# Optimization experiments

Measured on AMD Instinct MI355X. Metric: run time of the kernel, lower is better.

## Reference

```python
import jax, jax.numpy as jnp
import numpy as np

NEG = -1000000000.0

def setup_inputs() -> dict:
    key = jax.random.key(0)
    k1, k2, k3, k4 = jax.random.split(key, 4)
    B, S, D = 8, 4096, 256
    query = jax.random.normal(k1, (B, S, D), dtype=jnp.float32)
    k_ = jax.random.normal(k2, (B, S, D), dtype=jnp.float32)
    value = jax.random.normal(k3, (B, S, D), dtype=jnp.float32)
    mask = jax.random.bernoulli(k4, 0.1, (B, S, 1))  # True = masked
    return {"query": query, "key": k_, "value": value, "mask": mask}

def reference(query, key, value, mask):
    # a: [B,S,1] sum of squares of query; b: [B,S,1] for key
    a = jnp.sum(query * query, axis=-1, keepdims=True)
    b = jnp.sum(key * key, axis=-1, keepdims=True)
    # s1 = (K^T / b) @ V  -> [B, D, D]; divide each key row s by b_s
    s1 = jnp.einsum('bsd,bse->bde', key / b, value)
    # score = Q / a, masked rows set to -1e9
    score = query / a
    score = jnp.where(mask, NEG, score)
    s2 = jnp.einsum('bsd,bde->bse', score, s1)
    return s2 / query.shape[-1]
```

## Files before the change

kernel.cpp:

```cpp
#include <hip/hip_runtime.h>

#define BB 8
#define SS 4096
#define DD 256
#define NEGV -1000000000.0f

typedef float f32x4 __attribute__((ext_vector_type(4)));
typedef short s16x8 __attribute__((ext_vector_type(8)));

static __device__ __forceinline__ unsigned short f2bf(float x) {
  unsigned int u = __builtin_bit_cast(unsigned int, x);
  u += 0x7fffu + ((u >> 16) & 1u);
  return (unsigned short)(u >> 16);
}

__global__ __launch_bounds__(256) void prep_kernel(
    const float* __restrict__ Q, const float* __restrict__ K,
    const float* __restrict__ V, const int* __restrict__ mask,
    unsigned short* __restrict__ QS, unsigned short* __restrict__ KT,
    unsigned short* __restrict__ VT) {
  __shared__ unsigned short tile[DD * 68];
  const int b = blockIdx.y;
  const int s_base = blockIdx.x * 64;
  const int tid = threadIdx.x;
  const int w = tid >> 6;
  const int l = tid & 63;

  for (int it = 0; it < 16; ++it) {
    const int s = s_base + w * 16 + it;
    const size_t rowo = ((size_t)b * SS + s) * DD;
    const float4 q = *(const float4*)(Q + rowo + l * 4);
    float ss = q.x * q.x + q.y * q.y + q.z * q.z + q.w * q.w;
#pragma unroll
    for (int off = 32; off; off >>= 1) ss += __shfl_xor(ss, off);
    const int m = mask[b * SS + s];
    const float ca = m ? 0.0f : (1.0f / ss);
    const float aa = m ? NEGV : 0.0f;
    ushort4 o;
    o.x = f2bf(q.x * ca + aa);
    o.y = f2bf(q.y * ca + aa);
    o.z = f2bf(q.z * ca + aa);
    o.w = f2bf(q.w * ca + aa);
    *(ushort4*)(QS + rowo + l * 4) = o;
  }

  for (int it = 0; it < 16; ++it) {
    const int sl = w * 16 + it;
    const int s = s_base + sl;
    const float4 k = *(const float4*)(K + ((size_t)b * SS + s) * DD + l * 4);
    float ss = k.x * k.x + k.y * k.y + k.z * k.z + k.w * k.w;
#pragma unroll
    for (int off = 32; off; off >>= 1) ss += __shfl_xor(ss, off);
    const float binv = 1.0f / ss;
    tile[(l * 4 + 0) * 68 + sl] = f2bf(k.x * binv);
    tile[(l * 4 + 1) * 68 + sl] = f2bf(k.y * binv);
    tile[(l * 4 + 2) * 68 + sl] = f2bf(k.z * binv);
    tile[(l * 4 + 3) * 68 + sl] = f2bf(k.w * binv);
  }
  __syncthreads();
  {
    const size_t base = ((size_t)b * DD + tid) * SS + s_base;
#pragma unroll
    for (int c = 0; c < 8; ++c) {
      const uint2 a = *(const uint2*)(tile + tid * 68 + c * 8);
      const uint2 b2 = *(const uint2*)(tile + tid * 68 + c * 8 + 4);
      uint4 vv;
      vv.x = a.x; vv.y = a.y; vv.z = b2.x; vv.w = b2.y;
      *(uint4*)(KT + base + c * 8) = vv;
    }
  }
  __syncthreads();

  for (int it = 0; it < 16; ++it) {
    const int sl = w * 16 + it;
    const int s = s_base + sl;
    const float4 v = *(const float4*)(V + ((size_t)b * SS + s) * DD + l * 4);
    tile[(l * 4 + 0) * 68 + sl] = f2bf(v.x);
    tile[(l * 4 + 1) * 68 + sl] = f2bf(v.y);
    tile[(l * 4 + 2) * 68 + sl] = f2bf(v.z);
    tile[(l * 4 + 3) * 68 + sl] = f2bf(v.w);
  }
  __syncthreads();
  {
    const size_t base = ((size_t)b * DD + tid) * SS + s_base;
#pragma unroll
    for (int c = 0; c < 8; ++c) {
      const uint2 a = *(const uint2*)(tile + tid * 68 + c * 8);
      const uint2 b2 = *(const uint2*)(tile + tid * 68 + c * 8 + 4);
      uint4 vv;
      vv.x = a.x; vv.y = a.y; vv.z = b2.x; vv.w = b2.y;
      *(uint4*)(VT + base + c * 8) = vv;
    }
  }
}

__global__ __launch_bounds__(256) void p2_kernel(
    const unsigned short* __restrict__ KT, const unsigned short* __restrict__ VT,
    float* __restrict__ s1T) {
  __shared__ unsigned short vt_l[128 * 40];
  __shared__ unsigned short kt_l[128 * 40];
  const int b = blockIdx.z;
  const int d0 = (blockIdx.x & 1) * 128;
  const int e0 = (blockIdx.x >> 1) * 128;
  const int sbeg = blockIdx.y * 512;
  const int tid = threadIdx.x;
  const int w = tid >> 6, l = tid & 63;
  const int wr = w & 1, wc = w >> 1;
  const int quad = l >> 4, mr = l & 15;

  f32x4 acc[4][4];
#pragma unroll
  for (int i = 0; i < 4; ++i)
#pragma unroll
    for (int j = 0; j < 4; ++j) acc[i][j] = (f32x4){0.f, 0.f, 0.f, 0.f};

  const size_t vbase = ((size_t)b * DD + e0) * SS;
  const size_t kbase = ((size_t)b * DD + d0) * SS;

  for (int ks = 0; ks < 16; ++ks) {
    const int sc = sbeg + ks * 32;
#pragma unroll
    for (int it = 0; it < 2; ++it) {
      const int flat = it * 256 + tid;
      const int row = flat >> 2;
      const int c8 = (flat & 3) * 8;
      *(uint4*)(vt_l + row * 40 + c8) =
          *(const uint4*)(VT + vbase + (size_t)row * SS + sc + c8);
      *(uint4*)(kt_l + row * 40 + c8) =
          *(const uint4*)(KT + kbase + (size_t)row * SS + sc + c8);
    }
    __syncthreads();
    s16x8 af[4], bfr[4];
#pragma unroll
    for (int i = 0; i < 4; ++i)
      af[i] = *(const s16x8*)(vt_l + (wr * 64 + i * 16 + mr) * 40 + quad * 8);
#pragma unroll
    for (int j = 0; j < 4; ++j)
      bfr[j] = *(const s16x8*)(kt_l + (wc * 64 + j * 16 + mr) * 40 + quad * 8);
#pragma unroll
    for (int i = 0; i < 4; ++i)
#pragma unroll
      for (int j = 0; j < 4; ++j)
        acc[i][j] = __builtin_amdgcn_mfma_f32_16x16x32_bf16(af[i], bfr[j],
                                                            acc[i][j], 0, 0, 0);
    __syncthreads();
  }

#pragma unroll
  for (int i = 0; i < 4; ++i) {
    const int e = e0 + wr * 64 + i * 16 + quad * 4;
#pragma unroll
    for (int j = 0; j < 4; ++j) {
      const int d = d0 + wc * 64 + j * 16 + mr;
      float* p = s1T + ((size_t)b * DD + e) * DD + d;
#pragma unroll
      for (int r = 0; r < 4; ++r) atomicAdd(p + (size_t)r * DD, acc[i][j][r]);
    }
  }
}

__global__ __launch_bounds__(256) void p3_kernel(
    const unsigned short* __restrict__ QS, const float* __restrict__ s1T,
    float* __restrict__ out) {
  __shared__ unsigned short qs_l[128 * 40];
  __shared__ unsigned short s1_l[128 * 40];
  const int b = blockIdx.z;
  const int e0 = blockIdx.x * 128;
  const int s0 = blockIdx.y * 128;
  const int tid = threadIdx.x;
  const int w = tid >> 6, l = tid & 63;
  const int wr = w & 1, wc = w >> 1;
  const int quad = l >> 4, mr = l & 15;

  f32x4 acc[4][4];
#pragma unroll
  for (int i = 0; i < 4; ++i)
#pragma unroll
    for (int j = 0; j < 4; ++j) acc[i][j] = (f32x4){0.f, 0.f, 0.f, 0.f};

  for (int ks = 0; ks < 8; ++ks) {
    const int dc = ks * 32;
#pragma unroll
    for (int it = 0; it < 2; ++it) {
      const int flat = it * 256 + tid;
      const int row = flat >> 2;
      const int c8 = (flat & 3) * 8;
      *(uint4*)(qs_l + row * 40 + c8) =
          *(const uint4*)(QS + ((size_t)b * SS + s0 + row) * DD + dc + c8);
    }
#pragma unroll
    for (int it = 0; it < 4; ++it) {
      const int flat = it * 256 + tid;
      const int row = flat >> 3;
      const int c4 = (flat & 7) * 4;
      const float4 sv =
          *(const float4*)(s1T + ((size_t)b * DD + e0 + row) * DD + dc + c4);
      ushort4 o;
      o.x = f2bf(sv.x); o.y = f2bf(sv.y); o.z = f2bf(sv.z); o.w = f2bf(sv.w);
      *(ushort4*)(s1_l + row * 40 + c4) = o;
    }
    __syncthreads();
    s16x8 af[4], bfr[4];
#pragma unroll
    for (int i = 0; i < 4; ++i)
      af[i] = *(const s16x8*)(qs_l + (wr * 64 + i * 16 + mr) * 40 + quad * 8);
#pragma unroll
    for (int j = 0; j < 4; ++j)
      bfr[j] = *(const s16x8*)(s1_l + (wc * 64 + j * 16 + mr) * 40 + quad * 8);
#pragma unroll
    for (int i = 0; i < 4; ++i)
#pragma unroll
      for (int j = 0; j < 4; ++j)
        acc[i][j] = __builtin_amdgcn_mfma_f32_16x16x32_bf16(af[i], bfr[j],
                                                            acc[i][j], 0, 0, 0);
    __syncthreads();
  }

#pragma unroll
  for (int i = 0; i < 4; ++i) {
    const int s = s0 + wr * 64 + i * 16 + quad * 4;
#pragma unroll
    for (int j = 0; j < 4; ++j) {
      const int e = e0 + wc * 64 + j * 16 + mr;
      float* p = out + ((size_t)b * SS + s) * DD + e;
#pragma unroll
      for (int r = 0; r < 4; ++r) p[(size_t)r * DD] = acc[i][j][r] * (1.0f / DD);
    }
  }
}

extern "C" void kernel_launch(void* const* d_in, const int* in_sizes, int n_in,
                              void* d_out, int out_size, void* d_ws,
                              size_t ws_size, hipStream_t stream) {
  const float* Q = (const float*)d_in[0];
  const float* K = (const float*)d_in[1];
  const float* V = (const float*)d_in[2];
  const int* mask = (const int*)d_in[3];
  float* out = (float*)d_out;

  char* ws = (char*)d_ws;
  const size_t MB16 = (size_t)16 * 1024 * 1024;
  unsigned short* QS = (unsigned short*)(ws);
  unsigned short* KT = (unsigned short*)(ws + MB16);
  unsigned short* VT = (unsigned short*)(ws + 2 * MB16);
  float* s1T = (float*)(ws + 3 * MB16);

  hipMemsetAsync(s1T, 0, (size_t)BB * DD * DD * sizeof(float), stream);
  prep_kernel<<<dim3(SS / 64, BB), 256, 0, stream>>>(Q, K, V, mask, QS, KT, VT);
  p2_kernel<<<dim3(4, 8, BB), 256, 0, stream>>>(KT, VT, s1T);
  p3_kernel<<<dim3(2, SS / 128, BB), 256, 0, stream>>>(QS, s1T, out);
}
```

Measured before the change: 193.2 us.

## Split prep across Q/K/V blocks, replace atomics with split-K partials and reduce

```diff
diff --git a/kernel.cpp b/kernel.cpp
--- a/kernel.cpp
+++ b/kernel.cpp
@@ -19,90 +19,77 @@
     const float* __restrict__ V, const int* __restrict__ mask,
     unsigned short* __restrict__ QS, unsigned short* __restrict__ KT,
     unsigned short* __restrict__ VT) {
-  __shared__ unsigned short tile[DD * 68];
+  __shared__ unsigned short tile[DD * 34];
   const int b = blockIdx.y;
-  const int s_base = blockIdx.x * 64;
+  const int s0 = blockIdx.x * 32;
   const int tid = threadIdx.x;
-  const int w = tid >> 6;
-  const int l = tid & 63;
-
-  for (int it = 0; it < 16; ++it) {
-    const int s = s_base + w * 16 + it;
-    const size_t rowo = ((size_t)b * SS + s) * DD;
-    const float4 q = *(const float4*)(Q + rowo + l * 4);
-    float ss = q.x * q.x + q.y * q.y + q.z * q.z + q.w * q.w;
+  const int w = tid >> 6, l = tid & 63;
+
+  if (blockIdx.z == 0) {
+#pragma unroll
+    for (int it = 0; it < 8; ++it) {
+      const int s = s0 + w * 8 + it;
+      const size_t rowo = ((size_t)b * SS + s) * DD;
+      const float4 q = *(const float4*)(Q + rowo + l * 4);
+      float ss = q.x * q.x + q.y * q.y + q.z * q.z + q.w * q.w;
+#pragma unroll
+      for (int off = 32; off; off >>= 1) ss += __shfl_xor(ss, off);
+      const int m = mask[b * SS + s];
+      const float ca = m ? 0.0f : (1.0f / ss);
+      const float aa = m ? NEGV : 0.0f;
+      ushort4 o;
+      o.x = f2bf(q.x * ca + aa);
+      o.y = f2bf(q.y * ca + aa);
+      o.z = f2bf(q.z * ca + aa);
+      o.w = f2bf(q.w * ca + aa);
+      *(ushort4*)(QS + rowo + l * 4) = o;
+    }
+    return;
+  }
+
+  const int isK = (blockIdx.z == 1);
+  const float* __restrict__ src = isK ? K : V;
+  unsigned short* __restrict__ dst = isK ? KT : VT;
+
+#pragma unroll
+  for (int it = 0; it < 8; ++it) {
+    const int sl = w * 8 + it;
+    const size_t rowo = ((size_t)b * SS + s0 + sl) * DD;
+    const float v0 = src[rowo + l];
+    const float v1 = src[rowo + l + 64];
+    const float v2 = src[rowo + l + 128];
+    const float v3 = src[rowo + l + 192];
+    float ss = v0 * v0 + v1 * v1 + v2 * v2 + v3 * v3;
 #pragma unroll
     for (int off = 32; off; off >>= 1) ss += __shfl_xor(ss, off);
-    const int m = mask[b * SS + s];
-    const float ca = m ? 0.0f : (1.0f / ss);
-    const float aa = m ? NEGV : 0.0f;
-    ushort4 o;
-    o.x = f2bf(q.x * ca + aa);
-    o.y = f2bf(q.y * ca + aa);
-    o.z = f2bf(q.z * ca + aa);
-    o.w = f2bf(q.w * ca + aa);
-    *(ushort4*)(QS + rowo + l * 4) = o;
-  }
-
-  for (int it = 0; it < 16; ++it) {
-    const int sl = w * 16 + it;
-    const int s = s_base + sl;
-    const float4 k = *(const float4*)(K + ((size_t)b * SS + s) * DD + l * 4);
-    float ss = k.x * k.x + k.y * k.y + k.z * k.z + k.w * k.w;
-#pragma unroll
-    for (int off = 32; off; off >>= 1) ss += __shfl_xor(ss, off);
-    const float binv = 1.0f / ss;
-    tile[(l * 4 + 0) * 68 + sl] = f2bf(k.x * binv);
-    tile[(l * 4 + 1) * 68 + sl] = f2bf(k.y * binv);
-    tile[(l * 4 + 2) * 68 + sl] = f2bf(k.z * binv);
-    tile[(l * 4 + 3) * 68 + sl] = f2bf(k.w * binv);
+    const float sc = isK ? (1.0f / ss) : 1.0f;
+    tile[(l) * 34 + sl] = f2bf(v0 * sc);
+    tile[(l + 64) * 34 + sl] = f2bf(v1 * sc);
+    tile[(l + 128) * 34 + sl] = f2bf(v2 * sc);
+    tile[(l + 192) * 34 + sl] = f2bf(v3 * sc);
   }
   __syncthreads();
-  {
-    const size_t base = ((size_t)b * DD + tid) * SS + s_base;
-#pragma unroll
-    for (int c = 0; c < 8; ++c) {
-      const uint2 a = *(const uint2*)(tile + tid * 68 + c * 8);
-      const uint2 b2 = *(const uint2*)(tile + tid * 68 + c * 8 + 4);
-      uint4 vv;
-      vv.x = a.x; vv.y = a.y; vv.z = b2.x; vv.w = b2.y;
-      *(uint4*)(KT + base + c * 8) = vv;
-    }
-  }
-  __syncthreads();
-
-  for (int it = 0; it < 16; ++it) {
-    const int sl = w * 16 + it;
-    const int s = s_base + sl;
-    const float4 v = *(const float4*)(V + ((size_t)b * SS + s) * DD + l * 4);
-    tile[(l * 4 + 0) * 68 + sl] = f2bf(v.x);
-    tile[(l * 4 + 1) * 68 + sl] = f2bf(v.y);
-    tile[(l * 4 + 2) * 68 + sl] = f2bf(v.z);
-    tile[(l * 4 + 3) * 68 + sl] = f2bf(v.w);
-  }
-  __syncthreads();
-  {
-    const size_t base = ((size_t)b * DD + tid) * SS + s_base;
-#pragma unroll
-    for (int c = 0; c < 8; ++c) {
-      const uint2 a = *(const uint2*)(tile + tid * 68 + c * 8);
-      const uint2 b2 = *(const uint2*)(tile + tid * 68 + c * 8 + 4);
-      uint4 vv;
-      vv.x = a.x; vv.y = a.y; vv.z = b2.x; vv.w = b2.y;
-      *(uint4*)(VT + base + c * 8) = vv;
-    }
+  const size_t base = ((size_t)b * DD + tid) * SS + s0;
+#pragma unroll
+  for (int c = 0; c < 4; ++c) {
+    uint4 vv;
+    vv.x = *(const unsigned int*)(tile + tid * 34 + c * 8 + 0);
+    vv.y = *(const unsigned int*)(tile + tid * 34 + c * 8 + 2);
+    vv.z = *(const unsigned int*)(tile + tid * 34 + c * 8 + 4);
+    vv.w = *(const unsigned int*)(tile + tid * 34 + c * 8 + 6);
+    *(uint4*)(dst + base + c * 8) = vv;
   }
 }
 
 __global__ __launch_bounds__(256) void p2_kernel(
     const unsigned short* __restrict__ KT, const unsigned short* __restrict__ VT,
-    float* __restrict__ s1T) {
+    float* __restrict__ part, int nks) {
   __shared__ unsigned short vt_l[128 * 40];
   __shared__ unsigned short kt_l[128 * 40];
   const int b = blockIdx.z;
   const int d0 = (blockIdx.x & 1) * 128;
   const int e0 = (blockIdx.x >> 1) * 128;
-  const int sbeg = blockIdx.y * 512;
+  const int sbeg = blockIdx.y * nks * 32;
   const int tid = threadIdx.x;
   const int w = tid >> 6, l = tid & 63;
   const int wr = w & 1, wc = w >> 1;
@@ -117,7 +104,7 @@
   const size_t vbase = ((size_t)b * DD + e0) * SS;
   const size_t kbase = ((size_t)b * DD + d0) * SS;
 
-  for (int ks = 0; ks < 16; ++ks) {
+  for (int ks = 0; ks < nks; ++ks) {
     const int sc = sbeg + ks * 32;
 #pragma unroll
     for (int it = 0; it < 2; ++it) {
@@ -146,21 +133,36 @@
     __syncthreads();
   }
 
+  float* pb = part + (((size_t)blockIdx.y * BB + b) * DD) * DD;
 #pragma unroll
   for (int i = 0; i < 4; ++i) {
     const int e = e0 + wr * 64 + i * 16 + quad * 4;
 #pragma unroll
     for (int j = 0; j < 4; ++j) {
       const int d = d0 + wc * 64 + j * 16 + mr;
-      float* p = s1T + ((size_t)b * DD + e) * DD + d;
-#pragma unroll
-      for (int r = 0; r < 4; ++r) atomicAdd(p + (size_t)r * DD, acc[i][j][r]);
-    }
-  }
+      float* p = pb + (size_t)e * DD + d;
+#pragma unroll
+      for (int r = 0; r < 4; ++r) p[(size_t)r * DD] = acc[i][j][r];
+    }
+  }
+}
+
+__global__ __launch_bounds__(256) void reduce_kernel(
+    const float* __restrict__ part, unsigned short* __restrict__ s1b,
+    int split) {
+  const size_t i4 = ((size_t)blockIdx.x * 256 + threadIdx.x) * 4;
+  float ax = 0.f, ay = 0.f, az = 0.f, aw = 0.f;
+  for (int p = 0; p < split; ++p) {
+    const float4 v = *(const float4*)(part + (size_t)p * (BB * DD * DD) + i4);
+    ax += v.x; ay += v.y; az += v.z; aw += v.w;
+  }
+  ushort4 o;
+  o.x = f2bf(ax); o.y = f2bf(ay); o.z = f2bf(az); o.w = f2bf(aw);
+  *(ushort4*)(s1b + i4) = o;
 }
 
 __global__ __launch_bounds__(256) void p3_kernel(
-    const unsigned short* __restrict__ QS, const float* __restrict__ s1T,
+    const unsigned short* __restrict__ QS, const unsigned short* __restrict__ s1b,
     float* __restrict__ out) {
   __shared__ unsigned short qs_l[128 * 40];
   __shared__ unsigned short s1_l[128 * 40];
@@ -187,17 +189,8 @@
       const int c8 = (flat & 3) * 8;
       *(uint4*)(qs_l + row * 40 + c8) =
           *(const uint4*)(QS + ((size_t)b * SS + s0 + row) * DD + dc + c8);
-    }
-#pragma unroll
-    for (int it = 0; it < 4; ++it) {
-      const int flat = it * 256 + tid;
-      const int row = flat >> 3;
-      const int c4 = (flat & 7) * 4;
-      const float4 sv =
-          *(const float4*)(s1T + ((size_t)b * DD + e0 + row) * DD + dc + c4);
-      ushort4 o;
-      o.x = f2bf(sv.x); o.y = f2bf(sv.y); o.z = f2bf(sv.z); o.w = f2bf(sv.w);
-      *(ushort4*)(s1_l + row * 40 + c4) = o;
+      *(uint4*)(s1_l + row * 40 + c8) =
+          *(const uint4*)(s1b + ((size_t)b * DD + e0 + row) * DD + dc + c8);
     }
     __syncthreads();
     s16x8 af[4], bfr[4];
@@ -239,14 +232,20 @@
   float* out = (float*)d_out;
 
   char* ws = (char*)d_ws;
-  const size_t MB16 = (size_t)16 * 1024 * 1024;
+  const size_t MB = (size_t)1024 * 1024;
   unsigned short* QS = (unsigned short*)(ws);
-  unsigned short* KT = (unsigned short*)(ws + MB16);
-  unsigned short* VT = (unsigned short*)(ws + 2 * MB16);
-  float* s1T = (float*)(ws + 3 * MB16);
-
-  hipMemsetAsync(s1T, 0, (size_t)BB * DD * DD * sizeof(float), stream);
-  prep_kernel<<<dim3(SS / 64, BB), 256, 0, stream>>>(Q, K, V, mask, QS, KT, VT);
-  p2_kernel<<<dim3(4, 8, BB), 256, 0, stream>>>(KT, VT, s1T);
-  p3_kernel<<<dim3(2, SS / 128, BB), 256, 0, stream>>>(QS, s1T, out);
-}
+  unsigned short* KT = (unsigned short*)(ws + 16 * MB);
+  unsigned short* VT = (unsigned short*)(ws + 32 * MB);
+  float* part = (float*)(ws + 48 * MB);
+
+  const int split = (ws_size >= (size_t)84 * MB) ? 16 : 8;
+  const int nks = SS / (32 * split);
+  unsigned short* s1b =
+      (unsigned short*)(ws + 48 * MB + (size_t)split * 2 * MB);
+
+  prep_kernel<<<dim3(SS / 32, BB, 3), 256, 0, stream>>>(Q, K, V, mask, QS, KT,
+                                                        VT);
+  p2_kernel<<<dim3(4, split, BB), 256, 0, stream>>>(KT, VT, part, nks);
+  reduce_kernel<<<dim3(512), 256, 0, stream>>>(part, s1b, split);
+  p3_kernel<<<dim3(2, SS / 128, BB), 256, 0, stream>>>(QS, s1b, out);
+}
```

Measured after the change: 185.3 us. 4.1% less time.
